# Kernel optimization log

Measured on AMD Instinct MI355X. Metric: run time of the kernel, lower is better.

## Reference

```python
import jax, jax.numpy as jnp
import numpy as np

NU, NI, D, L = 100_000, 150_000, 64, 3
N = NU + NI
NNZ_A, NNZ_S = 2_000_000, 800_000


def _spmm(rows, cols, vals, X, n):
    # sparse [n, m] @ X[m, D] via gather + segment-sum (COO)
    return jax.ops.segment_sum(vals[:, None] * X[cols], rows, num_segments=n)


def _bilinear(x, c, W, b):
    # nn.Bilinear(D, D, 1) with second arg a single broadcast vector c: x_n^T W c + b
    return x @ (W @ c) + b[0]  # [Nu]


def setup_inputs() -> dict:
    key = jax.random.key(0)
    ks = jax.random.split(key, 20)
    f = jnp.float32
    inp = {
        "u1": jax.random.normal(ks[0], (NU, D), f) * 0.1,
        "u2": jax.random.normal(ks[1], (NU, D), f) * 0.1,
        "item_emb": jax.random.normal(ks[2], (NI, D), f) * 0.1,
        "Wi": jax.random.normal(ks[3], (D, D), f) * (1.0 / np.sqrt(D)),
        "Wc": jax.random.normal(ks[4], (D, D), f) * (1.0 / np.sqrt(D)),
        "Ws": jax.random.normal(ks[5], (D, 2 * D), f) * (1.0 / np.sqrt(2 * D)),
        "fk_W": jax.random.normal(ks[6], (D, D), f) * (1.0 / np.sqrt(D)),
        "fk_b": jax.random.normal(ks[7], (1,), f) * 0.01,
        "A_vals": jax.random.uniform(ks[8], (NNZ_A,), f) * 0.2,
        "A2_vals": jax.random.uniform(ks[9], (NNZ_A,), f) * 0.2,
        "S_vals": jax.random.uniform(ks[10], (NNZ_S,), f) * 0.2,
        "A_rows": jax.random.randint(ks[11], (NNZ_A,), 0, N, jnp.int32),
        "A_cols": jax.random.randint(ks[12], (NNZ_A,), 0, N, jnp.int32),
        "A2_rows": jax.random.randint(ks[13], (NNZ_A,), 0, N, jnp.int32),
        "A2_cols": jax.random.randint(ks[14], (NNZ_A,), 0, N, jnp.int32),
        "S_rows": jax.random.randint(ks[15], (NNZ_S,), 0, NU, jnp.int32),
        "S_cols": jax.random.randint(ks[16], (NNZ_S,), 0, NU, jnp.int32),
        "shuffle1": jax.random.permutation(ks[17], NU).astype(jnp.int32),
        "shuffle2": jax.random.permutation(ks[18], NU).astype(jnp.int32),
    }
    return inp


def reference(u1, u2, item_emb, Wi, Wc, Ws, fk_W, fk_b,
              A_vals, A2_vals, S_vals,
              A_rows, A_cols, A2_rows, A2_cols, S_rows, S_cols,
              shuffle1, shuffle2):
    # CLDS.computer, epoch >= 2000 branch. S1 = S2 = socialGraph2 in the source.
    users_emb0 = (u1 + u2) * 0.5
    all_emb = jnp.concatenate([users_emb0, item_emb])  # [N, D]
    u1_neg = u1[shuffle1]
    u2_neg = u2[shuffle2]
    embs = [all_emb]
    logits_true, logits_false = [], []
    for layer in range(L):
        rows, cols, vals = (A_rows, A_cols, A_vals) if layer == 0 else (A2_rows, A2_cols, A2_vals)
        agg = _spmm(rows, cols, vals, all_emb, N)          # [N, D]
        u_int, items_next = agg[:NU], agg[NU:]
        u_next = jnp.tanh(u_int @ Wi.T)                     # social_i + tanh
        all_emb = jnp.concatenate([u_next, items_next])
        u1_soc = jnp.tanh(_spmm(S_rows, S_cols, S_vals, u1, NU) @ Wc.T)
        u2_soc = jnp.tanh(_spmm(S_rows, S_cols, S_vals, u2, NU) @ Wc.T)
        u1_neg = jnp.tanh(_spmm(S_rows, S_cols, S_vals, u1_neg, NU) @ Wc.T)
        u2_neg = jnp.tanh(_spmm(S_rows, S_cols, S_vals, u2_neg, NU) @ Wc.T)
        c1 = jnp.mean(u1_soc, axis=0)
        c2 = jnp.mean(u2_soc, axis=0)
        sc1 = _bilinear(u2_soc, c1, fk_W, fk_b)
        sc2 = _bilinear(u1_soc, c2, fk_W, fk_b)
        sc3 = _bilinear(u2_neg, c1, fk_W, fk_b)
        sc4 = _bilinear(u1_neg, c2, fk_W, fk_b)
        logits_true.append(jnp.concatenate([sc1, sc2]))     # [2*NU]
        logits_false.append(jnp.concatenate([sc3, sc4]))
        u_comb = (u1_soc + u2_soc) * 0.5
        users = jnp.concatenate([u_next, u_comb], axis=1) @ Ws.T
        users = users / jnp.linalg.norm(users)              # global L2 norm, as in torch .norm(2)
        embs.append(jnp.concatenate([users, items_next]))
    final = jnp.mean(jnp.stack(embs, axis=1), axis=1)       # [N, D]
    # torch: stack([1,2Nu] x 2L, dim=2) -> [1,2Nu,2L] -> view(1,-1)
    logits = jnp.stack(logits_true + logits_false, axis=1).reshape(1, -1)
    return final[:NU], final[NU:], logits
```

## Files before the change

kernel.cpp:

```cpp
#include <hip/hip_runtime.h>

#define NU 100000
#define NI 150000
#define NTOT 250000
#define DD 64
#define NNZ_A 2000000
#define NNZ_S 800000
#define SCAN_CHUNK 2048

typedef unsigned int uint;
typedef unsigned short ushort;

#define LB __launch_bounds__(256, 4)

#define RFL(x) __builtin_amdgcn_readfirstlane(x)

__device__ __forceinline__ uint f2bf_bits(float x) {
  uint a = __float_as_uint(x);
  return (a + 0x7fffu + ((a >> 16) & 1u)) >> 16;
}
__device__ __forceinline__ ushort f2bf(float x) { return (ushort)f2bf_bits(x); }
__device__ __forceinline__ float bf2f(ushort h) { return __uint_as_float(((uint)h) << 16); }
__device__ __forceinline__ uint pack_bf16x2(float lo, float hi) {
  return f2bf_bits(lo) | (f2bf_bits(hi) << 16);
}
__device__ __forceinline__ float unpk_lo(uint p) { return __uint_as_float(p << 16); }
__device__ __forceinline__ float unpk_hi(uint p) { return __uint_as_float(p & 0xffff0000u); }

__device__ __forceinline__ float tanh_fast(float x) {
  float e = __expf(2.0f * x);
  return 1.0f - __fdividef(2.0f, e + 1.0f);
}

__device__ __forceinline__ void gemm64x2_b(float aA, float aB,
                                           const float* __restrict__ Wt,
                                           volatile float* __restrict__ ab, int lane,
                                           float& oA, float& oB) {
  asm volatile("s_waitcnt lgkmcnt(0)" ::: "memory");
  __builtin_amdgcn_sched_barrier(0);
  ab[lane] = aA;
  ab[64 + lane] = aB;
  asm volatile("s_waitcnt lgkmcnt(0)" ::: "memory");
  __builtin_amdgcn_sched_barrier(0);
  float sA = 0.f, sB = 0.f;
#pragma unroll 4
  for (int k0 = 0; k0 < 64; k0 += 4) {
    float4 a4 = *(const float4*)(const float*)(ab + k0);
    float4 b4 = *(const float4*)(const float*)(ab + 64 + k0);
#pragma unroll
    for (int u = 0; u < 4; ++u) {
      float wk = Wt[(k0 + u) * 65 + lane];
      sA = fmaf(((const float*)&a4)[u], wk, sA);
      sB = fmaf(((const float*)&b4)[u], wk, sB);
    }
  }
  oA = sA; oB = sB;
}

__device__ __forceinline__ void gemm64x4_b(float a0, float a1, float a2, float a3,
                                           const float* __restrict__ Wt,
                                           volatile float* __restrict__ ab, int lane,
                                           float& o0, float& o1, float& o2, float& o3) {
  asm volatile("s_waitcnt lgkmcnt(0)" ::: "memory");
  __builtin_amdgcn_sched_barrier(0);
  ab[lane] = a0;
  ab[64 + lane] = a1;
  ab[128 + lane] = a2;
  ab[192 + lane] = a3;
  asm volatile("s_waitcnt lgkmcnt(0)" ::: "memory");
  __builtin_amdgcn_sched_barrier(0);
  float s0 = 0.f, s1 = 0.f, s2 = 0.f, s3 = 0.f;
#pragma unroll 4
  for (int k0 = 0; k0 < 64; k0 += 4) {
    float4 x0 = *(const float4*)(const float*)(ab + k0);
    float4 x1 = *(const float4*)(const float*)(ab + 64 + k0);
    float4 x2 = *(const float4*)(const float*)(ab + 128 + k0);
    float4 x3 = *(const float4*)(const float*)(ab + 192 + k0);
#pragma unroll
    for (int u = 0; u < 4; ++u) {
      float wk = Wt[(k0 + u) * 65 + lane];
      s0 = fmaf(((const float*)&x0)[u], wk, s0);
      s1 = fmaf(((const float*)&x1)[u], wk, s1);
      s2 = fmaf(((const float*)&x2)[u], wk, s2);
      s3 = fmaf(((const float*)&x3)[u], wk, s3);
    }
  }
  o0 = s0; o1 = s1; o2 = s2; o3 = s3;
}

__device__ __forceinline__ float gemm64x1_b(float a, const float* __restrict__ Wt,
                                            volatile float* __restrict__ ab, int lane) {
  asm volatile("s_waitcnt lgkmcnt(0)" ::: "memory");
  __builtin_amdgcn_sched_barrier(0);
  ab[lane] = a;
  asm volatile("s_waitcnt lgkmcnt(0)" ::: "memory");
  __builtin_amdgcn_sched_barrier(0);
  float s = 0.f;
#pragma unroll 4
  for (int k0 = 0; k0 < 64; k0 += 4) {
    float4 a4 = *(const float4*)(const float*)(ab + k0);
#pragma unroll
    for (int u = 0; u < 4; ++u)
      s = fmaf(((const float*)&a4)[u], Wt[(k0 + u) * 65 + lane], s);
  }
  return s;
}

__device__ __forceinline__ void stage_wt(const float* __restrict__ W, float* __restrict__ Wt) {
  for (int idx = threadIdx.x; idx < 64 * 64; idx += blockDim.x)
    Wt[(idx & 63) * 65 + (idx >> 6)] = W[idx];
  __syncthreads();
}

__global__ void k_init(const float* __restrict__ u1, const float* __restrict__ u2,
                       const float* __restrict__ item, ushort* __restrict__ emb_bf,
                       float* __restrict__ out_final) {
  int idx = blockIdx.x * blockDim.x + threadIdx.x;
  const int tot = NTOT * DD;
  const int nu = NU * DD;
  for (; idx < tot; idx += gridDim.x * blockDim.x) {
    float v;
    if (idx < nu) v = 0.5f * (u1[idx] + u2[idx]);
    else          v = item[idx - nu];
    emb_bf[idx] = f2bf(v);
    out_final[idx] = 0.25f * v;
  }
}

__global__ void k_hist_rank(const int* __restrict__ rows, int* __restrict__ cnt,
                            int* __restrict__ rank, int nnz) {
  int tid = blockIdx.x * blockDim.x + threadIdx.x;
  int gsz = gridDim.x * blockDim.x;
  for (int b = tid; b < nnz; b += gsz * 8) {
#pragma unroll
    for (int u = 0; u < 8; ++u) {
      int i = b + u * gsz;
      if (i < nnz) rank[i] = atomicAdd(&cnt[rows[i]], 1);
    }
  }
}

__global__ void k_scan1(const int* __restrict__ cnt, int* __restrict__ bsum, int n) {
  __shared__ int sdata[256];
  int base = blockIdx.x * SCAN_CHUNK;
  int s = 0;
#pragma unroll
  for (int k = 0; k < 8; ++k) {
    int i = base + threadIdx.x * 8 + k;
    s += (i < n) ? cnt[i] : 0;
  }
  sdata[threadIdx.x] = s;
  __syncthreads();
  for (int off = 128; off > 0; off >>= 1) {
    if (threadIdx.x < off) sdata[threadIdx.x] += sdata[threadIdx.x + off];
    __syncthreads();
  }
  if (threadIdx.x == 0) bsum[blockIdx.x] = sdata[0];
}

__global__ void k_scan2(int* bsum, int nb) {
  __shared__ int sdata[256];
  int v = (threadIdx.x < nb) ? bsum[threadIdx.x] : 0;
  sdata[threadIdx.x] = v;
  __syncthreads();
  for (int off = 1; off < 256; off <<= 1) {
    int t = (threadIdx.x >= (unsigned)off) ? sdata[threadIdx.x - off] : 0;
    __syncthreads();
    sdata[threadIdx.x] += t;
    __syncthreads();
  }
  if (threadIdx.x < nb) bsum[threadIdx.x] = sdata[threadIdx.x] - v;
}

__global__ void k_scan3(const int* __restrict__ cnt, const int* __restrict__ bsum,
                        int* __restrict__ rowptr, int n, int nnz) {
  __shared__ int sdata[256];
  int base = blockIdx.x * SCAN_CHUNK;
  int loc[8];
  int s = 0;
#pragma unroll
  for (int k = 0; k < 8; ++k) {
    int i = base + threadIdx.x * 8 + k;
    loc[k] = (i < n) ? cnt[i] : 0;
    s += loc[k];
  }
  sdata[threadIdx.x] = s;
  __syncthreads();
  for (int off = 1; off < 256; off <<= 1) {
    int t = (threadIdx.x >= (unsigned)off) ? sdata[threadIdx.x - off] : 0;
    __syncthreads();
    sdata[threadIdx.x] += t;
    __syncthreads();
  }
  int pre = bsum[blockIdx.x] + sdata[threadIdx.x] - s;
#pragma unroll
  for (int k = 0; k < 8; ++k) {
    int i = base + threadIdx.x * 8 + k;
    if (i < n) { rowptr[i] = pre; pre += loc[k]; }
  }
  if (blockIdx.x == 0 && threadIdx.x == 0) rowptr[n] = nnz;
}

__global__ void k_scatter2(const int* __restrict__ rows, const int* __restrict__ cols,
                           const float* __restrict__ vals, const int* __restrict__ ptr,
                           const int* __restrict__ rank, int2* __restrict__ cv, int nnz) {
  int tid = blockIdx.x * blockDim.x + threadIdx.x;
  int gsz = gridDim.x * blockDim.x;
  for (int b = tid; b < nnz; b += gsz * 8) {
#pragma unroll
    for (int u = 0; u < 8; ++u) {
      int i = b + u * gsz;
      if (i < nnz) {
        int r = rows[i];
        cv[ptr[r] + rank[i]] = make_int2(cols[i], __float_as_int(vals[i]));
      }
    }
  }
}

__global__ LB void k_transform(const float* __restrict__ u1, const float* __restrict__ u2,
                               const float* __restrict__ Wc, uint* __restrict__ SOCPt) {
  __shared__ float Wt[64 * 65];
  __shared__ float AB[4][128];
  stage_wt(Wc, Wt);
  int lane = threadIdx.x & 63;
  volatile float* ab = AB[threadIdx.x >> 6];
  int wid = (blockIdx.x * blockDim.x + threadIdx.x) >> 6;
  int nw = (gridDim.x * blockDim.x) >> 6;
  for (int i = wid; i < NU; i += nw) {
    float a1 = u1[(size_t)i * DD + lane];
    float a2 = u2[(size_t)i * DD + lane];
    float o1, o2;
    gemm64x2_b(a1, a2, Wt, ab, lane, o1, o2);
    SOCPt[(size_t)i * DD + lane] = pack_bf16x2(o1, o2);
  }
}

__global__ void k_negmap(const uint* __restrict__ SOCPt, const int* __restrict__ s1,
                         const int* __restrict__ s2, uint2* __restrict__ QUADP) {
  int idx = blockIdx.x * blockDim.x + threadIdx.x;
  const int tot = NU * DD;
  for (; idx < tot; idx += gridDim.x * blockDim.x) {
    int i = idx >> 6, j = idx & 63;
    uint soc = SOCPt[idx];
    uint lo = SOCPt[(size_t)s1[i] * DD + j];
    uint hi = SOCPt[(size_t)s2[i] * DD + j];
    QUADP[idx] = make_uint2(soc, (lo & 0xffffu) | (hi & 0xffff0000u));
  }
}

__global__ LB void k_quadS(const int* __restrict__ rowptr, const int2* __restrict__ cv,
                           const uint2* __restrict__ QUADP, const float* __restrict__ Wc,
                           ushort* __restrict__ u1s, ushort* __restrict__ u2s,
                           ushort* __restrict__ n1o, ushort* __restrict__ n2o,
                           uint* __restrict__ NEGPa) {
  __shared__ float Wt[64 * 65];
  __shared__ float AB[4][128];
  stage_wt(Wc, Wt);
  int lane = threadIdx.x & 63;
  volatile float* ab = AB[threadIdx.x >> 6];
  int wid = (blockIdx.x * blockDim.x + threadIdx.x) >> 6;
  int nw = (gridDim.x * blockDim.x) >> 6;
  for (int r = wid; r < NU; r += nw) {
    int start = RFL(rowptr[r]);
    int n = RFL(rowptr[r + 1]) - start;
    float a1 = 0.f, a2 = 0.f, a3 = 0.f, a4 = 0.f;
    for (int k = 0; k < n; k += 8) {
      int2 e[8];
#pragma unroll
      for (int u = 0; u < 8; ++u) e[u] = cv[start + k + u];
      uint2 q[8];
#pragma unroll
      for (int u = 0; u < 8; ++u)
        q[u] = QUADP[(size_t)(uint)e[u].x * 64u + (uint)lane];
#pragma unroll
      for (int u = 0; u < 8; ++u) {
        float sv = (k + u < n) ? __int_as_float(e[u].y) : 0.f;
        a1 = fmaf(sv, unpk_lo(q[u].x), a1);
        a2 = fmaf(sv, unpk_hi(q[u].x), a2);
        a3 = fmaf(sv, unpk_lo(q[u].y), a3);
        a4 = fmaf(sv, unpk_hi(q[u].y), a4);
      }
    }
    float t1 = tanh_fast(a1), t2 = tanh_fast(a2), t3 = tanh_fast(a3), t4 = tanh_fast(a4);
    u1s[(size_t)r * DD + lane] = f2bf(t1);
    u2s[(size_t)r * DD + lane] = f2bf(t2);
    n1o[(size_t)r * DD + lane] = f2bf(t3);
    n2o[(size_t)r * DD + lane] = f2bf(t4);
    float o3, o4;
    gemm64x2_b(t3, t4, Wt, ab, lane, o3, o4);
    NEGPa[(size_t)r * DD + lane] = pack_bf16x2(o3, o4);
  }
}

__global__ LB void k_dualS(const int* __restrict__ rowptr, const int2* __restrict__ cv,
                           const uint* __restrict__ T, const float* __restrict__ Wc,
                           const float* __restrict__ wva, const float* __restrict__ wvb,
                           const float* __restrict__ fkb, float* __restrict__ out_logits,
                           int slot, uint* __restrict__ Tnext) {
  __shared__ float Wt[64 * 65];
  __shared__ float AB[4][256];
  stage_wt(Wc, Wt);
  int lane = threadIdx.x & 63;
  volatile float* ab = AB[threadIdx.x >> 6];
  int wid = (blockIdx.x * blockDim.x + threadIdx.x) >> 6;
  int nw = (gridDim.x * blockDim.x) >> 6;
  float b = fkb[0];
  float wa = wva[lane], wb = wvb[lane];
  for (int r = wid * 2; r < NU; r += nw * 2) {
    int s0 = RFL(rowptr[r]);
    int sm = RFL(rowptr[r + 1]);
    int s1e = RFL(rowptr[r + 2]);
    int n0 = sm - s0, n1 = s1e - sm;
    int kmax = max(n0, n1);
    float a0A = 0.f, a0B = 0.f, a1A = 0.f, a1B = 0.f;
    for (int k = 0; k < kmax; k += 8) {
      int b0 = (k < n0) ? s0 + k : s0;
      int b1 = (k < n1) ? sm + k : sm;
      int2 e0[8], e1[8];
#pragma unroll
      for (int u = 0; u < 8; ++u) e0[u] = cv[b0 + u];
#pragma unroll
      for (int u = 0; u < 8; ++u) e1[u] = cv[b1 + u];
      uint q0[8], q1[8];
#pragma unroll
      for (int u = 0; u < 8; ++u)
        q0[u] = T[(size_t)(uint)e0[u].x * 64u + (uint)lane];
#pragma unroll
      for (int u = 0; u < 8; ++u)
        q1[u] = T[(size_t)(uint)e1[u].x * 64u + (uint)lane];
#pragma unroll
      for (int u = 0; u < 8; ++u) {
        float sv0 = (k + u < n0) ? __int_as_float(e0[u].y) : 0.f;
        float sv1 = (k + u < n1) ? __int_as_float(e1[u].y) : 0.f;
        a0A = fmaf(sv0, unpk_lo(q0[u]), a0A);
        a0B = fmaf(sv0, unpk_hi(q0[u]), a0B);
        a1A = fmaf(sv1, unpk_lo(q1[u]), a1A);
        a1B = fmaf(sv1, unpk_hi(q1[u]), a1B);
      }
    }
    float t0a = tanh_fast(a0A), t0b = tanh_fast(a0B);
    float t1a = tanh_fast(a1A), t1b = tanh_fast(a1B);
    float p0a = t0a * wa, p0b = t0b * wb, p1a = t1a * wa, p1b = t1b * wb;
#pragma unroll
    for (int off = 32; off > 0; off >>= 1) {
      p0a += __shfl_xor(p0a, off);
      p0b += __shfl_xor(p0b, off);
      p1a += __shfl_xor(p1a, off);
      p1b += __shfl_xor(p1b, off);
    }
    if (lane == 0) {
      out_logits[(size_t)(NU + r) * 6 + slot] = p0a + b;
      out_logits[(size_t)r * 6 + slot] = p0b + b;
      out_logits[(size_t)(NU + r + 1) * 6 + slot] = p1a + b;
      out_logits[(size_t)(r + 1) * 6 + slot] = p1b + b;
    }
    if (Tnext) {
      float o0a, o0b, o1a, o1b;
      gemm64x4_b(t0a, t0b, t1a, t1b, Wt, ab, lane, o0a, o0b, o1a, o1b);
      Tnext[(size_t)r * DD + lane] = pack_bf16x2(o0a, o0b);
      Tnext[(size_t)(r + 1) * DD + lane] = pack_bf16x2(o1a, o1b);
    }
  }
}

__global__ LB void k_spmm_fusedA2(const int* __restrict__ rowptr, const int2* __restrict__ cv,
                                  const ushort* __restrict__ X, const float* __restrict__ W,
                                  ushort* __restrict__ embNext, float* __restrict__ outF) {
  __shared__ float Wt[64 * 65];
  __shared__ float AB[4][256];
  stage_wt(W, Wt);
  int lane = threadIdx.x & 63;
  volatile float* ab = AB[threadIdx.x >> 6];
  int wid = (blockIdx.x * blockDim.x + threadIdx.x) >> 6;
  int nw = (gridDim.x * blockDim.x) >> 6;
  for (int r = wid * 4; r < NTOT; r += nw * 4) {
    int sp[5];
#pragma unroll
    for (int i = 0; i < 5; ++i) sp[i] = RFL(rowptr[r + i]);
    int n0 = sp[1] - sp[0], n1 = sp[2] - sp[1];
    int n2 = sp[3] - sp[2], n3 = sp[4] - sp[3];
    int kmax = max(max(n0, n1), max(n2, n3));
    float acc0 = 0.f, acc1 = 0.f, acc2 = 0.f, acc3 = 0.f;
    for (int k = 0; k < kmax; k += 8) {
      int b0 = (k < n0) ? sp[0] + k : sp[0];
      int b1 = (k < n1) ? sp[1] + k : sp[1];
      int b2 = (k < n2) ? sp[2] + k : sp[2];
      int b3 = (k < n3) ? sp[3] + k : sp[3];
      int2 e0[8], e1[8], e2[8], e3[8];
#pragma unroll
      for (int u = 0; u < 8; ++u) e0[u] = cv[b0 + u];
#pragma unroll
      for (int u = 0; u < 8; ++u) e1[u] = cv[b1 + u];
#pragma unroll
      for (int u = 0; u < 8; ++u) e2[u] = cv[b2 + u];
#pragma unroll
      for (int u = 0; u < 8; ++u) e3[u] = cv[b3 + u];
      uint h0[8], h1[8], h2[8], h3[8];
#pragma unroll
      for (int u = 0; u < 8; ++u)
        h0[u] = X[(size_t)(uint)e0[u].x * 64u + (uint)lane];
#pragma unroll
      for (int u = 0; u < 8; ++u)
        h1[u] = X[(size_t)(uint)e1[u].x * 64u + (uint)lane];
#pragma unroll
      for (int u = 0; u < 8; ++u)
        h2[u] = X[(size_t)(uint)e2[u].x * 64u + (uint)lane];
#pragma unroll
      for (int u = 0; u < 8; ++u)
        h3[u] = X[(size_t)(uint)e3[u].x * 64u + (uint)lane];
#pragma unroll
      for (int u = 0; u < 8; ++u) {
        float sv0 = (k + u < n0) ? __int_as_float(e0[u].y) : 0.f;
        float sv1 = (k + u < n1) ? __int_as_float(e1[u].y) : 0.f;
        float sv2 = (k + u < n2) ? __int_as_float(e2[u].y) : 0.f;
        float sv3 = (k + u < n3) ? __int_as_float(e3[u].y) : 0.f;
        acc0 = fmaf(sv0, __uint_as_float(h0[u] << 16), acc0);
        acc1 = fmaf(sv1, __uint_as_float(h1[u] << 16), acc1);
        acc2 = fmaf(sv2, __uint_as_float(h2[u] << 16), acc2);
        acc3 = fmaf(sv3, __uint_as_float(h3[u] << 16), acc3);
      }
    }
    if (r < NU) {
      float o0, o1, o2, o3;
      gemm64x4_b(acc0, acc1, acc2, acc3, Wt, ab, lane, o0, o1, o2, o3);
      embNext[(size_t)r * DD + lane] = f2bf(tanh_fast(o0));
      embNext[(size_t)(r + 1) * DD + lane] = f2bf(tanh_fast(o1));
      embNext[(size_t)(r + 2) * DD + lane] = f2bf(tanh_fast(o2));
      embNext[(size_t)(r + 3) * DD + lane] = f2bf(tanh_fast(o3));
    } else {
      embNext[(size_t)r * DD + lane] = f2bf(acc0);
      embNext[(size_t)(r + 1) * DD + lane] = f2bf(acc1);
      embNext[(size_t)(r + 2) * DD + lane] = f2bf(acc2);
      embNext[(size_t)(r + 3) * DD + lane] = f2bf(acc3);
      outF[(size_t)r * DD + lane] += 0.25f * acc0;
      outF[(size_t)(r + 1) * DD + lane] += 0.25f * acc1;
      outF[(size_t)(r + 2) * DD + lane] += 0.25f * acc2;
      outF[(size_t)(r + 3) * DD + lane] += 0.25f * acc3;
    }
  }
}

__global__ void k_colsum2(const ushort* __restrict__ x1, const ushort* __restrict__ x2,
                          float* __restrict__ c1, float* __restrict__ c2) {
  int lane = threadIdx.x & 63;
  int wid = (blockIdx.x * blockDim.x + threadIdx.x) >> 6;
  int nw = (gridDim.x * blockDim.x) >> 6;
  float a1 = 0.f, a2 = 0.f;
  for (int i = wid; i < NU; i += nw) {
    a1 += bf2f(x1[(size_t)i * DD + lane]);
    a2 += bf2f(x2[(size_t)i * DD + lane]);
  }
  atomicAdd(&c1[lane], a1);
  atomicAdd(&c2[lane], a2);
}

__global__ void k_wvec(const float* __restrict__ fkW, const float* __restrict__ c1r,
                       const float* __restrict__ c2r, float* __restrict__ w1,
                       float* __restrict__ w2) {
  int j = threadIdx.x;
  float a1 = 0.f, a2 = 0.f;
  for (int k = 0; k < 64; ++k) {
    float w = fkW[j * 64 + k];
    a1 += w * c1r[k];
    a2 += w * c2r[k];
  }
  w1[j] = a1 * (1.0f / NU);
  w2[j] = a2 * (1.0f / NU);
}

__global__ void k_logits4(const ushort* __restrict__ u1s, const ushort* __restrict__ u2s,
                          const ushort* __restrict__ n1o, const ushort* __restrict__ n2o,
                          const float* __restrict__ w1, const float* __restrict__ w2,
                          const float* __restrict__ fkb, float* __restrict__ out_logits) {
  int lane = threadIdx.x & 63;
  int wid = (blockIdx.x * blockDim.x + threadIdx.x) >> 6;
  int nw = (gridDim.x * blockDim.x) >> 6;
  float b = fkb[0];
  for (int i = wid; i < 2 * NU; i += nw) {
    bool lo = i < NU;
    int r = lo ? i : i - NU;
    const ushort* xs = lo ? u2s : u1s;
    const ushort* xn = lo ? n2o : n1o;
    const float* wv = lo ? w1 : w2;
    float wvl = wv[lane];
    float ps = bf2f(xs[(size_t)r * DD + lane]) * wvl;
    float pn = bf2f(xn[(size_t)r * DD + lane]) * wvl;
#pragma unroll
    for (int off = 32; off > 0; off >>= 1) {
      ps += __shfl_xor(ps, off);
      pn += __shfl_xor(pn, off);
    }
    if (lane == 0) {
      float vs = ps + b;
      out_logits[(size_t)i * 6 + 0] = vs;
      out_logits[(size_t)i * 6 + 1] = vs;
      out_logits[(size_t)i * 6 + 2] = vs;
      out_logits[(size_t)i * 6 + 3] = pn + b;
    }
  }
}

__global__ LB void k_comb_gemm(const ushort* __restrict__ u1s, const ushort* __restrict__ u2s,
                               const float* __restrict__ Ws, ushort* __restrict__ UC) {
  __shared__ float Wt[64 * 65];
  __shared__ float AB[4][128];
  for (int idx = threadIdx.x; idx < 64 * 64; idx += blockDim.x)
    Wt[(idx & 63) * 65 + (idx >> 6)] = Ws[(idx >> 6) * 128 + 64 + (idx & 63)];
  __syncthreads();
  int lane = threadIdx.x & 63;
  volatile float* ab = AB[threadIdx.x >> 6];
  int wid = (blockIdx.x * blockDim.x + threadIdx.x) >> 6;
  int nw = (gridDim.x * blockDim.x) >> 6;
  for (int i = wid; i < NU; i += nw) {
    float c = 0.5f * (bf2f(u1s[(size_t)i * DD + lane]) + bf2f(u2s[(size_t)i * DD + lane]));
    UC[(size_t)i * DD + lane] = f2bf(gemm64x1_b(c, Wt, ab, lane));
  }
}

__global__ LB void k_users(const ushort* __restrict__ u_next, const ushort* __restrict__ uc,
                           const float* __restrict__ Ws, float* __restrict__ users_raw,
                           float* __restrict__ sumsq) {
  __shared__ float Wt[64 * 65];
  __shared__ float AB[4][128];
  for (int idx = threadIdx.x; idx < 64 * 64; idx += blockDim.x)
    Wt[(idx & 63) * 65 + (idx >> 6)] = Ws[(idx >> 6) * 128 + (idx & 63)];
  __syncthreads();
  int lane = threadIdx.x & 63;
  volatile float* ab = AB[threadIdx.x >> 6];
  int wid = (blockIdx.x * blockDim.x + threadIdx.x) >> 6;
  int nw = (gridDim.x * blockDim.x) >> 6;
  float ss = 0.f;
  for (int i = wid; i < NU; i += nw) {
    float va = bf2f(u_next[(size_t)i * DD + lane]);
    float acc = bf2f(uc[(size_t)i * DD + lane]) + gemm64x1_b(va, Wt, ab, lane);
    users_raw[(size_t)i * DD + lane] = acc;
    ss += acc * acc;
  }
#pragma unroll
  for (int off = 32; off > 0; off >>= 1) ss += __shfl_xor(ss, off);
  if (lane == 0) atomicAdd(sumsq, ss);
}

__global__ void k_users_acc(const float* __restrict__ users_raw,
                            const float* __restrict__ sumsq, float* __restrict__ out_final) {
  float scale = 0.25f / sqrtf(*sumsq);
  int idx = blockIdx.x * blockDim.x + threadIdx.x;
  for (; idx < NU * DD; idx += gridDim.x * blockDim.x)
    out_final[idx] += users_raw[idx] * scale;
}

extern "C" void kernel_launch(void* const* d_in, const int* in_sizes, int n_in,
                              void* d_out, int out_size, void* d_ws, size_t ws_size,
                              hipStream_t stream) {
  const float* u1      = (const float*)d_in[0];
  const float* u2      = (const float*)d_in[1];
  const float* item    = (const float*)d_in[2];
  const float* Wi      = (const float*)d_in[3];
  const float* Wc      = (const float*)d_in[4];
  const float* Ws      = (const float*)d_in[5];
  const float* fk_W    = (const float*)d_in[6];
  const float* fk_b    = (const float*)d_in[7];
  const float* A_vals  = (const float*)d_in[8];
  const float* A2_vals = (const float*)d_in[9];
  const float* S_vals  = (const float*)d_in[10];
  const int*   A_rows  = (const int*)d_in[11];
  const int*   A_cols  = (const int*)d_in[12];
  const int*   A2_rows = (const int*)d_in[13];
  const int*   A2_cols = (const int*)d_in[14];
  const int*   S_rows  = (const int*)d_in[15];
  const int*   S_cols  = (const int*)d_in[16];
  const int*   sh1     = (const int*)d_in[17];
  const int*   sh2     = (const int*)d_in[18];

  float* ws = (float*)d_ws;
  ushort* embA_bf = (ushort*)ws;
  ushort* embB_bf = (ushort*)(ws + 8000000);
  uint2*  QUADP   = (uint2*)(ws + 16000000);
  uint*   NEGPb   = (uint*)(ws + 16000000);
  float*  uraw    = ws + 22400000;
  uint*   NEGPa   = (uint*)(ws + 28800000);
  ushort* u1s     = (ushort*)(ws + 35200000);
  ushort* u2s     = (ushort*)(ws + 38400000);
  int2*   cvA2    = (int2*)(ws + 35200000);
  int*    ptrA2   = (int*)(ws + 39200016);
  uint*   SOCPt   = (uint*)(ws + 41600000);
  ushort* n1o     = (ushort*)(ws + 41600000);
  ushort* UCb     = (ushort*)(ws + 41600000);
  ushort* n2o     = (ushort*)(ws + 44800000);
  int2*   cvA     = (int2*)(ws + 48000000);
  int2*   cvS     = (int2*)(ws + 52000016);
  int*    ptrA    = (int*)(ws + 53600032);
  int*    ptrS    = ptrA + (NTOT + 1);
  int*    cnt     = ptrS + (NU + 1);
  int*    bsum    = cnt + NTOT;
  float*  c1r     = (float*)(bsum + 256);
  float*  c2r     = c1r + 64;
  float*  w1      = c2r + 64;
  float*  w2      = w1 + 64;
  float*  sumsq   = w2 + 64;
  int*    rank    = (int*)(ws + 54200580);

  float* out        = (float*)d_out;
  float* out_logits = out + (size_t)NTOT * DD;

  auto build = [&](const int* rows, const int* cols, const float* vals,
                   int n, int nnz, int* ptr, int2* cv) {
    int nb = (n + SCAN_CHUNK - 1) / SCAN_CHUNK;
    int gb = (nnz + 2047) / 2048;
    hipMemsetAsync(cnt, 0, (size_t)n * sizeof(int), stream);
    k_hist_rank<<<gb, 256, 0, stream>>>(rows, cnt, rank, nnz);
    k_scan1<<<nb, 256, 0, stream>>>(cnt, bsum, n);
    k_scan2<<<1, 256, 0, stream>>>(bsum, nb);
    k_scan3<<<nb, 256, 0, stream>>>(cnt, bsum, ptr, n, nnz);
    k_scatter2<<<gb, 256, 0, stream>>>(rows, cols, vals, ptr, rank, cv, nnz);
    hipMemsetAsync(cv + nnz, 0, 8 * sizeof(int2), stream);
  };

  build(S_rows, S_cols, S_vals, NU, NNZ_S, ptrS, cvS);
  build(A_rows, A_cols, A_vals, NTOT, NNZ_A, ptrA, cvA);

  hipMemsetAsync(c1r, 0, 128 * sizeof(float), stream);
  k_init<<<2048, 256, 0, stream>>>(u1, u2, item, embA_bf, out);
  k_transform<<<1024, 256, 0, stream>>>(u1, u2, Wc, SOCPt);
  k_negmap<<<1024, 256, 0, stream>>>(SOCPt, sh1, sh2, QUADP);

  k_quadS<<<2048, 256, 0, stream>>>(ptrS, cvS, QUADP, Wc,
                                    u1s, u2s, n1o, n2o, NEGPa);
  k_colsum2<<<256, 256, 0, stream>>>(u1s, u2s, c1r, c2r);
  k_wvec<<<1, 64, 0, stream>>>(fk_W, c1r, c2r, w1, w2);
  k_logits4<<<1024, 256, 0, stream>>>(u1s, u2s, n1o, n2o, w1, w2, fk_b, out_logits);
  k_comb_gemm<<<1024, 256, 0, stream>>>(u1s, u2s, Ws, UCb);

  build(A2_rows, A2_cols, A2_vals, NTOT, NNZ_A, ptrA2, cvA2);

  ushort* embCur = embA_bf;
  ushort* embNext = embB_bf;
  for (int l = 0; l < 3; ++l) {
    const int* pA = (l == 0) ? ptrA : ptrA2;
    const int2* cA = (l == 0) ? cvA : cvA2;

    k_spmm_fusedA2<<<4096, 256, 0, stream>>>(pA, cA, embCur, Wi, embNext, out);

    if (l == 1)
      k_dualS<<<2048, 256, 0, stream>>>(ptrS, cvS, NEGPa, Wc, w2, w1, fk_b,
                                        out_logits, 4, NEGPb);
    else if (l == 2)
      k_dualS<<<2048, 256, 0, stream>>>(ptrS, cvS, NEGPb, Wc, w2, w1, fk_b,
                                        out_logits, 5, (uint*)nullptr);

    hipMemsetAsync(sumsq, 0, sizeof(float), stream);
    k_users<<<1024, 256, 0, stream>>>(embNext, UCb, Ws, uraw, sumsq);
    k_users_acc<<<2048, 256, 0, stream>>>(uraw, sumsq, out);

    { ushort* t = embCur; embCur = embNext; embNext = t; }
  }
}
```

Before: 1.487 ms.

## Batch S and A CSR builds into shared launches and fuse user init into transform

The CSR construction for the social graph S and adjacency A now runs as combined histogram, scan and scatter kernels, with block ranges split between the two graphs. This halves the launch count and lets the small S build fill the GPU alongside A. The user half of the embedding init moves into k_transform, which already reads u1/u2, so k_init only handles items. Separate rank/count buffers are carved out of workspace that is later reused as QUADP, and the trailing memset on cv is folded into the scatter kernel.

```diff
diff --git a/kernel.cpp b/kernel.cpp
--- a/kernel.cpp
+++ b/kernel.cpp
@@ -7,12 +7,15 @@
 #define NNZ_A 2000000
 #define NNZ_S 800000
 #define SCAN_CHUNK 2048
+#define NBS 49
+#define NBA 123
+#define GBS 391
+#define GBA 977
 
 typedef unsigned int uint;
 typedef unsigned short ushort;
 
 #define LB __launch_bounds__(256, 4)
-
 #define RFL(x) __builtin_amdgcn_readfirstlane(x)
 
 __device__ __forceinline__ uint f2bf_bits(float x) {
@@ -112,25 +115,22 @@
   __syncthreads();
 }
 
-__global__ void k_init(const float* __restrict__ u1, const float* __restrict__ u2,
-                       const float* __restrict__ item, ushort* __restrict__ emb_bf,
-                       float* __restrict__ out_final) {
+__global__ void k_init_items(const float* __restrict__ item, ushort* __restrict__ emb_bf,
+                             float* __restrict__ out_final) {
   int idx = blockIdx.x * blockDim.x + threadIdx.x;
-  const int tot = NTOT * DD;
+  const int tot = NI * DD;
   const int nu = NU * DD;
   for (; idx < tot; idx += gridDim.x * blockDim.x) {
-    float v;
-    if (idx < nu) v = 0.5f * (u1[idx] + u2[idx]);
-    else          v = item[idx - nu];
-    emb_bf[idx] = f2bf(v);
-    out_final[idx] = 0.25f * v;
-  }
-}
-
-__global__ void k_hist_rank(const int* __restrict__ rows, int* __restrict__ cnt,
-                            int* __restrict__ rank, int nnz) {
-  int tid = blockIdx.x * blockDim.x + threadIdx.x;
-  int gsz = gridDim.x * blockDim.x;
+    float v = item[idx];
+    emb_bf[nu + idx] = f2bf(v);
+    out_final[nu + idx] = 0.25f * v;
+  }
+}
+
+__device__ __forceinline__ void hist_body(const int* rows, int* cnt, int* rank,
+                                          int nnz, int bid, int nb) {
+  int tid = bid * 256 + threadIdx.x;
+  int gsz = nb * 256;
   for (int b = tid; b < nnz; b += gsz * 8) {
 #pragma unroll
     for (int u = 0; u < 8; ++u) {
@@ -140,9 +140,22 @@
   }
 }
 
-__global__ void k_scan1(const int* __restrict__ cnt, int* __restrict__ bsum, int n) {
+__global__ void k_hist1(const int* __restrict__ rows, int* __restrict__ cnt,
+                        int* __restrict__ rank, int nnz) {
+  hist_body(rows, cnt, rank, nnz, blockIdx.x, gridDim.x);
+}
+
+__global__ void k_hist2(const int* __restrict__ rowsS, int* __restrict__ cntS,
+                        int* __restrict__ rankS,
+                        const int* __restrict__ rowsA, int* __restrict__ cntA,
+                        int* __restrict__ rankA) {
+  if ((int)blockIdx.x < GBS) hist_body(rowsS, cntS, rankS, NNZ_S, blockIdx.x, GBS);
+  else                       hist_body(rowsA, cntA, rankA, NNZ_A, blockIdx.x - GBS, GBA);
+}
+
+__device__ __forceinline__ void scan1_body(const int* cnt, int* bsum, int n, int bid) {
   __shared__ int sdata[256];
-  int base = blockIdx.x * SCAN_CHUNK;
+  int base = bid * SCAN_CHUNK;
   int s = 0;
 #pragma unroll
   for (int k = 0; k < 8; ++k) {
@@ -155,10 +168,20 @@
     if (threadIdx.x < off) sdata[threadIdx.x] += sdata[threadIdx.x + off];
     __syncthreads();
   }
-  if (threadIdx.x == 0) bsum[blockIdx.x] = sdata[0];
-}
-
-__global__ void k_scan2(int* bsum, int nb) {
+  if (threadIdx.x == 0) bsum[bid] = sdata[0];
+}
+
+__global__ void k_scan1(const int* __restrict__ cnt, int* __restrict__ bsum, int n) {
+  scan1_body(cnt, bsum, n, blockIdx.x);
+}
+
+__global__ void k_scan1_2(const int* __restrict__ cntS, int* __restrict__ bsumS,
+                          const int* __restrict__ cntA, int* __restrict__ bsumA) {
+  if ((int)blockIdx.x < NBS) scan1_body(cntS, bsumS, NU, blockIdx.x);
+  else                       scan1_body(cntA, bsumA, NTOT, blockIdx.x - NBS);
+}
+
+__device__ __forceinline__ void scan2_body(int* bsum, int nb) {
   __shared__ int sdata[256];
   int v = (threadIdx.x < nb) ? bsum[threadIdx.x] : 0;
   sdata[threadIdx.x] = v;
@@ -172,10 +195,17 @@
   if (threadIdx.x < nb) bsum[threadIdx.x] = sdata[threadIdx.x] - v;
 }
 
-__global__ void k_scan3(const int* __restrict__ cnt, const int* __restrict__ bsum,
-                        int* __restrict__ rowptr, int n, int nnz) {
+__global__ void k_scan2(int* bsum, int nb) { scan2_body(bsum, nb); }
+
+__global__ void k_scan2_2(int* bsumS, int* bsumA) {
+  if (blockIdx.x == 0) scan2_body(bsumS, NBS);
+  else                 scan2_body(bsumA, NBA);
+}
+
+__device__ __forceinline__ void scan3_body(const int* cnt, const int* bsum,
+                                           int* rowptr, int n, int nnz, int bid) {
   __shared__ int sdata[256];
-  int base = blockIdx.x * SCAN_CHUNK;
+  int base = bid * SCAN_CHUNK;
   int loc[8];
   int s = 0;
 #pragma unroll
@@ -192,20 +222,34 @@
     sdata[threadIdx.x] += t;
     __syncthreads();
   }
-  int pre = bsum[blockIdx.x] + sdata[threadIdx.x] - s;
+  int pre = bsum[bid] + sdata[threadIdx.x] - s;
 #pragma unroll
   for (int k = 0; k < 8; ++k) {
     int i = base + threadIdx.x * 8 + k;
     if (i < n) { rowptr[i] = pre; pre += loc[k]; }
   }
-  if (blockIdx.x == 0 && threadIdx.x == 0) rowptr[n] = nnz;
-}
-
-__global__ void k_scatter2(const int* __restrict__ rows, const int* __restrict__ cols,
-                           const float* __restrict__ vals, const int* __restrict__ ptr,
-                           const int* __restrict__ rank, int2* __restrict__ cv, int nnz) {
-  int tid = blockIdx.x * blockDim.x + threadIdx.x;
-  int gsz = gridDim.x * blockDim.x;
+  if (bid == 0 && threadIdx.x == 0) rowptr[n] = nnz;
+}
+
+__global__ void k_scan3(const int* __restrict__ cnt, const int* __restrict__ bsum,
+                        int* __restrict__ rowptr, int n, int nnz) {
+  scan3_body(cnt, bsum, rowptr, n, nnz, blockIdx.x);
+}
+
+__global__ void k_scan3_2(const int* __restrict__ cntS, const int* __restrict__ bsumS,
+                          int* __restrict__ ptrS,
+                          const int* __restrict__ cntA, const int* __restrict__ bsumA,
+                          int* __restrict__ ptrA) {
+  if ((int)blockIdx.x < NBS) scan3_body(cntS, bsumS, ptrS, NU, NNZ_S, blockIdx.x);
+  else                       scan3_body(cntA, bsumA, ptrA, NTOT, NNZ_A, blockIdx.x - NBS);
+}
+
+__device__ __forceinline__ void scatter_body(const int* rows, const int* cols,
+                                             const float* vals, const int* ptr,
+                                             const int* rank, int2* cv, int nnz,
+                                             int bid, int nb) {
+  int tid = bid * 256 + threadIdx.x;
+  int gsz = nb * 256;
   for (int b = tid; b < nnz; b += gsz * 8) {
 #pragma unroll
     for (int u = 0; u < 8; ++u) {
@@ -216,10 +260,30 @@
       }
     }
   }
+  if (bid == 0 && threadIdx.x < 8) cv[nnz + threadIdx.x] = make_int2(0, 0);
+}
+
+__global__ void k_scatter1(const int* __restrict__ rows, const int* __restrict__ cols,
+                           const float* __restrict__ vals, const int* __restrict__ ptr,
+                           const int* __restrict__ rank, int2* __restrict__ cv, int nnz) {
+  scatter_body(rows, cols, vals, ptr, rank, cv, nnz, blockIdx.x, gridDim.x);
+}
+
+__global__ void k_scatter2_2(const int* __restrict__ rowsS, const int* __restrict__ colsS,
+                             const float* __restrict__ valsS, const int* __restrict__ ptrS,
+                             const int* __restrict__ rankS, int2* __restrict__ cvS,
+                             const int* __restrict__ rowsA, const int* __restrict__ colsA,
+                             const float* __restrict__ valsA, const int* __restrict__ ptrA,
+                             const int* __restrict__ rankA, int2* __restrict__ cvA) {
+  if ((int)blockIdx.x < GBS)
+    scatter_body(rowsS, colsS, valsS, ptrS, rankS, cvS, NNZ_S, blockIdx.x, GBS);
+  else
+    scatter_body(rowsA, colsA, valsA, ptrA, rankA, cvA, NNZ_A, blockIdx.x - GBS, GBA);
 }
 
 __global__ LB void k_transform(const float* __restrict__ u1, const float* __restrict__ u2,
-                               const float* __restrict__ Wc, uint* __restrict__ SOCPt) {
+                               const float* __restrict__ Wc, uint* __restrict__ SOCPt,
+                               ushort* __restrict__ emb_bf, float* __restrict__ out_final) {
   __shared__ float Wt[64 * 65];
   __shared__ float AB[4][128];
   stage_wt(Wc, Wt);
@@ -230,6 +294,9 @@
   for (int i = wid; i < NU; i += nw) {
     float a1 = u1[(size_t)i * DD + lane];
     float a2 = u2[(size_t)i * DD + lane];
+    float v = 0.5f * (a1 + a2);
+    emb_bf[(size_t)i * DD + lane] = f2bf(v);
+    out_final[(size_t)i * DD + lane] = 0.25f * v;
     float o1, o2;
     gemm64x2_b(a1, a2, Wt, ab, lane, o1, o2);
     SOCPt[(size_t)i * DD + lane] = pack_bf16x2(o1, o2);
@@ -577,6 +644,12 @@
   ushort* embA_bf = (ushort*)ws;
   ushort* embB_bf = (ushort*)(ws + 8000000);
   uint2*  QUADP   = (uint2*)(ws + 16000000);
+  int*    rankS2  = (int*)(ws + 16000000);
+  int*    rankA   = (int*)(ws + 16800000);
+  int*    cntS    = (int*)(ws + 18800000);
+  int*    cntA    = (int*)(ws + 18900000);
+  int*    bsumS   = (int*)(ws + 19150000);
+  int*    bsumA   = (int*)(ws + 19150256);
   uint*   NEGPb   = (uint*)(ws + 16000000);
   float*  uraw    = ws + 22400000;
   uint*   NEGPa   = (uint*)(ws + 28800000);
@@ -604,35 +677,35 @@
   float* out        = (float*)d_out;
   float* out_logits = out + (size_t)NTOT * DD;
 
-  auto build = [&](const int* rows, const int* cols, const float* vals,
-                   int n, int nnz, int* ptr, int2* cv) {
-    int nb = (n + SCAN_CHUNK - 1) / SCAN_CHUNK;
-    int gb = (nnz + 2047) / 2048;
-    hipMemsetAsync(cnt, 0, (size_t)n * sizeof(int), stream);
-    k_hist_rank<<<gb, 256, 0, stream>>>(rows, cnt, rank, nnz);
-    k_scan1<<<nb, 256, 0, stream>>>(cnt, bsum, n);
-    k_scan2<<<1, 256, 0, stream>>>(bsum, nb);
-    k_scan3<<<nb, 256, 0, stream>>>(cnt, bsum, ptr, n, nnz);
-    k_scatter2<<<gb, 256, 0, stream>>>(rows, cols, vals, ptr, rank, cv, nnz);
-    hipMemsetAsync(cv + nnz, 0, 8 * sizeof(int2), stream);
-  };
-
-  build(S_rows, S_cols, S_vals, NU, NNZ_S, ptrS, cvS);
-  build(A_rows, A_cols, A_vals, NTOT, NNZ_A, ptrA, cvA);
+  hipMemsetAsync(cntS, 0, 350000 * sizeof(int), stream);
+  k_hist2<<<GBS + GBA, 256, 0, stream>>>(S_rows, cntS, rankS2, A_rows, cntA, rankA);
+  k_scan1_2<<<NBS + NBA, 256, 0, stream>>>(cntS, bsumS, cntA, bsumA);
+  k_scan2_2<<<2, 256, 0, stream>>>(bsumS, bsumA);
+  k_scan3_2<<<NBS + NBA, 256, 0, stream>>>(cntS, bsumS, ptrS, cntA, bsumA, ptrA);
+  k_scatter2_2<<<GBS + GBA, 256, 0, stream>>>(S_rows, S_cols, S_vals, ptrS, rankS2, cvS,
+                                              A_rows, A_cols, A_vals, ptrA, rankA, cvA);
 
   hipMemsetAsync(c1r, 0, 128 * sizeof(float), stream);
-  k_init<<<2048, 256, 0, stream>>>(u1, u2, item, embA_bf, out);
-  k_transform<<<1024, 256, 0, stream>>>(u1, u2, Wc, SOCPt);
+  k_init_items<<<1024, 256, 0, stream>>>(item, embA_bf, out);
+  k_transform<<<1024, 256, 0, stream>>>(u1, u2, Wc, SOCPt, embA_bf, out);
   k_negmap<<<1024, 256, 0, stream>>>(SOCPt, sh1, sh2, QUADP);
 
-  k_quadS<<<2048, 256, 0, stream>>>(ptrS, cvS, QUADP, Wc,
-                                    u1s, u2s, n1o, n2o, NEGPa);
+  k_quadS<<<2048, 256, 0, stream>>>(ptrS, cvS, QUADP, Wc, u1s, u2s, n1o, n2o, NEGPa);
   k_colsum2<<<256, 256, 0, stream>>>(u1s, u2s, c1r, c2r);
   k_wvec<<<1, 64, 0, stream>>>(fk_W, c1r, c2r, w1, w2);
   k_logits4<<<1024, 256, 0, stream>>>(u1s, u2s, n1o, n2o, w1, w2, fk_b, out_logits);
   k_comb_gemm<<<1024, 256, 0, stream>>>(u1s, u2s, Ws, UCb);
 
-  build(A2_rows, A2_cols, A2_vals, NTOT, NNZ_A, ptrA2, cvA2);
+  {
+    int nb = (NTOT + SCAN_CHUNK - 1) / SCAN_CHUNK;
+    int gb = (NNZ_A + 2047) / 2048;
+    hipMemsetAsync(cnt, 0, (size_t)NTOT * sizeof(int), stream);
+    k_hist1<<<gb, 256, 0, stream>>>(A2_rows, cnt, rank, NNZ_A);
+    k_scan1<<<nb, 256, 0, stream>>>(cnt, bsum, NTOT);
+    k_scan2<<<1, 256, 0, stream>>>(bsum, nb);
+    k_scan3<<<nb, 256, 0, stream>>>(cnt, bsum, ptrA2, NTOT, NNZ_A);
+    k_scatter1<<<gb, 256, 0, stream>>>(A2_rows, A2_cols, A2_vals, ptrA2, rank, cvA2, NNZ_A);
+  }
 
   ushort* embCur = embA_bf;
   ushort* embNext = embB_bf;
```

Result: no change. 1.461 ms (-1.7%).
